# Kernel tuning notes

Measured on AMD Instinct MI355X. Metric: run time of the kernel, lower is better.

## Reference

```python
import jax, jax.numpy as jnp
import numpy as np

N = 50000        # n_nodes
E = 640000       # n_edges
D = 128          # d_model (in_dim == out_dim)
H = 8            # num_heads
DH = D // H      # head dim = 16
EPS = 1e-5


def _batchnorm(x, g, b):
    # BatchNorm1d, training-mode batch statistics (biased variance)
    mu = jnp.mean(x, axis=0)
    var = jnp.mean((x - mu) ** 2, axis=0)
    return (x - mu) * jax.lax.rsqrt(var + EPS) * g + b


def setup_inputs() -> dict:
    key = jax.random.key(0)
    ks = jax.random.split(key, 16)
    s = 0.05
    h = jax.random.normal(ks[0], (N, D), jnp.float32)
    src = jax.random.randint(ks[1], (E,), 0, N)
    # guarantee every node has >= 1 incoming edge (avoids z == 0)
    dst = jnp.concatenate([jnp.arange(N), jax.random.randint(ks[2], (E - N,), 0, N)])
    return {
        "h": h,
        "src": src,
        "dst": dst,
        "WQ": jax.random.normal(ks[3], (D, D), jnp.float32) * s,
        "WK": jax.random.normal(ks[4], (D, D), jnp.float32) * s,
        "WV": jax.random.normal(ks[5], (D, D), jnp.float32) * s,
        "WO": jax.random.normal(ks[6], (D, D), jnp.float32) * s,
        "bO": jnp.zeros((D,), jnp.float32),
        "W1": jax.random.normal(ks[7], (2 * D, D), jnp.float32) * s,
        "b1": jnp.zeros((2 * D,), jnp.float32),
        "W2": jax.random.normal(ks[8], (D, 2 * D), jnp.float32) * s,
        "b2": jnp.zeros((D,), jnp.float32),
        "bn1_g": jnp.ones((D,), jnp.float32),
        "bn1_b": jnp.zeros((D,), jnp.float32),
        "bn2_g": jnp.ones((D,), jnp.float32),
        "bn2_b": jnp.zeros((D,), jnp.float32),
    }


def reference(h, src, dst, WQ, WK, WV, WO, bO, W1, b1, W2, b2, bn1_g, bn1_b, bn2_g, bn2_b):
    n = h.shape[0]
    # projections -> [N, H, DH]
    Q = (h @ WQ.T).reshape(n, H, DH)
    K = (h @ WK.T).reshape(n, H, DH)
    V = (h @ WV.T).reshape(n, H, DH)
    # per-edge score: sum(K[src] * Q[dst]) -> [E, H]; clamp/exp (scaled_exp)
    score = jnp.sum(K[src] * Q[dst], axis=-1) / np.sqrt(DH)
    score = jnp.exp(jnp.clip(score, -5.0, 5.0))
    # scatter-sum weighted values and normalizers to destination nodes
    wV = jax.ops.segment_sum(V[src] * score[..., None], dst, num_segments=n)  # [N,H,DH]
    z = jax.ops.segment_sum(score, dst, num_segments=n)                       # [N,H]
    attn = (wV / z[..., None]).reshape(n, D)
    # O projection + residual + BN1
    h1 = _batchnorm(h + (attn @ WO.T + bO), bn1_g, bn1_b)
    # FFN + residual + BN2
    f = jax.nn.relu(h1 @ W1.T + b1) @ W2.T + b2
    return _batchnorm(h1 + f, bn2_g, bn2_b)
```

## Files before the change

### kernel.cpp

```cpp
#include <hip/hip_runtime.h>
#include <math.h>


#define ND128 16384
typedef _Float16 f16;
typedef __attribute__((ext_vector_type(8))) _Float16 h8;
typedef __attribute__((ext_vector_type(4))) _Float16 h4;
typedef __attribute__((ext_vector_type(2))) _Float16 h2;
typedef __attribute__((ext_vector_type(4))) float f4;
typedef __attribute__((ext_vector_type(2))) float ff2;

__device__ __forceinline__ float fast_exp2(float x) {
#if __has_builtin(__builtin_amdgcn_exp2f)
    return __builtin_amdgcn_exp2f(x);
#else
    return exp2f(x);
#endif
}

template <int CTRL>
__device__ __forceinline__ float dppadd(float x) {
    int t = __builtin_amdgcn_update_dpp(0, __float_as_int(x), CTRL, 0xF, 0xF, false);
    return x + __int_as_float(t);
}
__device__ __forceinline__ float wsum8(float p) {
    p = dppadd<0xB1>(p);
    p = dppadd<0x4E>(p);
    p = dppadd<0x141>(p);
    return p;
}

__device__ __forceinline__ ff2 fp8x2_dec_sw(unsigned v) {
    ff2 r;
    unsigned b0 = v & 0xffu, b1 = (v >> 8) & 0xffu;
    {
        unsigned e = (b0 >> 3) & 15u, m = b0 & 7u;
        float x = e ? __uint_as_float(((e + 120u) << 23) | (m << 20)) : (float)m * 0.001953125f;
        r.x = (b0 & 0x80u) ? -x : x;
    }
    {
        unsigned e = (b1 >> 3) & 15u, m = b1 & 7u;
        float x = e ? __uint_as_float(((e + 120u) << 23) | (m << 20)) : (float)m * 0.001953125f;
        r.y = (b1 & 0x80u) ? -x : x;
    }
    return r;
}

__device__ __forceinline__ ff2 dec_lo(unsigned v) {
#if __has_builtin(__builtin_amdgcn_cvt_pk_f32_fp8)
    return __builtin_amdgcn_cvt_pk_f32_fp8((int)v, false);
#else
    return fp8x2_dec_sw(v & 0xffffu);
#endif
}
__device__ __forceinline__ ff2 dec_hi(unsigned v) {
#if __has_builtin(__builtin_amdgcn_cvt_pk_f32_fp8)
    return __builtin_amdgcn_cvt_pk_f32_fp8((int)v, true);
#else
    return fp8x2_dec_sw((v >> 16) & 0xffffu);
#endif
}

#if !__has_builtin(__builtin_amdgcn_cvt_pk_fp8_f32)
__device__ __forceinline__ unsigned char fp8_1(float f) {
    float a = fabsf(f);
    unsigned sg = (__float_as_uint(f) >> 31) << 7;
    if (a >= 448.f) return (unsigned char)(sg | 0x7E);
    if (a < 0.0009765625f) return (unsigned char)sg;
    int E; float m = frexpf(a, &E);
    if (E - 1 < -6) {
        int q = (int)rintf(a * 512.f);
        if (q > 7) return (unsigned char)(sg | 0x08);
        return (unsigned char)(sg | q);
    }
    int q = (int)rintf(m * 16.f);
    if (q == 16) { q = 8; E += 1; }
    int Ef = E - 1 + 7;
    if (Ef > 15) return (unsigned char)(sg | 0x7E);
    return (unsigned char)(sg | (Ef << 3) | (q - 8));
}
#endif

__device__ __forceinline__ unsigned short fp8_pack2(float a0, float a1) {
#if __has_builtin(__builtin_amdgcn_cvt_pk_fp8_f32)
    int pk = __builtin_amdgcn_cvt_pk_fp8_f32(a0, a1, 0, false);
    return (unsigned short)(pk & 0xffff);
#else
    return (unsigned short)((unsigned)fp8_1(a0) | ((unsigned)fp8_1(a1) << 8));
#endif
}

__global__ __launch_bounds__(256) void k_prep_hist(
    const float* __restrict__ WQ, const float* __restrict__ WK,
    const float* __restrict__ WV, const float* __restrict__ WO,
    const float* __restrict__ W2,
    f16* __restrict__ Wqb, f16* __restrict__ Wkb,
    f16* __restrict__ Wvb, f16* __restrict__ Wob, f16* __restrict__ W2b,
    int* __restrict__ cursor, const int* __restrict__ dst,
    int N, int E, int nhb)
{
    const int tid = threadIdx.x;
    if (blockIdx.x < (unsigned)nhb) {
        int e = blockIdx.x * 256 + tid;
        if (e < E) atomicAdd(&cursor[dst[e]], 1);
        return;
    }
    const int ws = blockIdx.x - nhb;
    const float* Wsrc; f16* dstw; int K, base;
    if (ws < 4) {
        Wsrc = ws == 0 ? WQ : ws == 1 ? WK : ws == 2 ? WV : WO;
        dstw = ws == 0 ? Wqb : ws == 1 ? Wkb : ws == 2 ? Wvb : Wob;
        K = 128; base = 0;
    } else {
        Wsrc = W2; dstw = W2b; K = 256; base = (ws - 4) * 2048;
    }
#pragma unroll
    for (int it = 0; it < 8; ++it) {
        int cid = base + it * 256 + tid;
        int lane = cid & 63;
        int kb, nt;
        if (K == 128) { kb = (cid >> 6) & 3; nt = cid >> 8; }
        else          { kb = (cid >> 6) & 7; nt = cid >> 9; }
        int row = nt * 16 + (lane & 15);
        int col = kb * 32 + (lane >> 4) * 8;
        const float* pp = Wsrc + (size_t)row * K + col;
        f16 o8[8];
#pragma unroll
        for (int j = 0; j < 8; ++j) o8[j] = (f16)pp[j];
        *(h8*)(dstw + (size_t)cid * 8) = *(const h8*)o8;
    }
}

__global__ __launch_bounds__(512) void k_qkvf(
    const float* __restrict__ h, f16* __restrict__ hb,
    const f16* __restrict__ Wqb, const f16* __restrict__ Wkb,
    const f16* __restrict__ Wvb,
    f16* __restrict__ Qb, unsigned char* __restrict__ KV8,
    const int* __restrict__ cursor, int* __restrict__ bsum, int N, int nsb)
{
    __shared__ f16 sA[ND128];
    __shared__ int ws8[8];
    const int tid = threadIdx.x;
    if (blockIdx.x < (unsigned)nsb) {
        int base = blockIdx.x * 2048 + tid * 4;
        int s = 0;
#pragma unroll
        for (int j = 0; j < 4; ++j) {
            int idx = base + j;
            if (idx < N) s += cursor[idx];
        }
#pragma unroll
        for (int off = 32; off; off >>= 1) s += __shfl_down(s, off, 64);
        if ((tid & 63) == 0) ws8[tid >> 6] = s;
        __syncthreads();
        if (tid == 0) {
            int r = 0;
#pragma unroll
            for (int k = 0; k < 8; ++k) r += ws8[k];
            bsum[blockIdx.x] = r;
        }
        return;
    }
    const int slab = blockIdx.x - nsb;
#pragma unroll
    for (int it = 0; it < 4; ++it) {
        int cid = it * 512 + tid;
        int lane = cid & 63;
        int m = (cid >> 6) & 7;
        int kb = cid >> 9;
        int row = slab * 128 + m * 16 + (lane & 15);
        int col = kb * 32 + (lane >> 4) * 8;
        f16 o8[8];
        if (row < N) {
            const float* pp = h + (size_t)row * 128 + col;
            float4 f0 = *(const float4*)pp;
            float4 f1 = *(const float4*)(pp + 4);
            o8[0] = (f16)f0.x; o8[1] = (f16)f0.y; o8[2] = (f16)f0.z; o8[3] = (f16)f0.w;
            o8[4] = (f16)f1.x; o8[5] = (f16)f1.y; o8[6] = (f16)f1.z; o8[7] = (f16)f1.w;
        } else {
#pragma unroll
            for (int j = 0; j < 8; ++j) o8[j] = (f16)0.f;
        }
        h8 v = *(const h8*)o8;
        *(h8*)(hb + (size_t)slab * ND128 + (size_t)cid * 8) = v;
        *(h8*)(sA + (size_t)cid * 8) = v;
    }
    __syncthreads();

    const int w2 = tid >> 6, lane = tid & 63;
    const int rl = lane & 15, quad = lane >> 4;
#pragma unroll
    for (int oidx = 0; oidx < 3; ++oidx) {
        const f16* __restrict__ Wb = oidx == 0 ? Wqb : oidx == 1 ? Wkb : Wvb;
        h8 bfr[4];
#pragma unroll
        for (int kb = 0; kb < 4; ++kb)
            bfr[kb] = *(const h8*)(Wb + (size_t)((w2 * 4 + kb) * 64 + lane) * 8);

        f4 acc[8];
        f4 zero = {0.f, 0.f, 0.f, 0.f};
#pragma unroll
        for (int m = 0; m < 8; ++m) acc[m] = zero;
#pragma unroll
        for (int m = 0; m < 8; ++m) {
#pragma unroll
            for (int kb = 0; kb < 4; ++kb) {
                h8 a = *(const h8*)(sA + (size_t)((kb * 8 + m) * 64 + lane) * 8);
                acc[m] = __builtin_amdgcn_mfma_f32_16x16x32_f16(bfr[kb], a, acc[m], 0, 0, 0);
            }
        }
        if (oidx == 0) {
#pragma unroll
            for (int m = 0; m < 8; ++m) {
                int gr = slab * 128 + m * 16 + rl;
                if (gr < N) {
                    h4 o;
                    o[0] = (f16)acc[m][0]; o[1] = (f16)acc[m][1];
                    o[2] = (f16)acc[m][2]; o[3] = (f16)acc[m][3];
                    *(h4*)(Qb + (size_t)gr * 128 + w2 * 16 + quad * 4) = o;
                }
            }
        } else {
            const int koff = (oidx == 2) ? 2 : 0;
#pragma unroll
            for (int m = 0; m < 8; ++m) {
                int gr = slab * 128 + m * 16 + rl;
                if (gr < N) {
                    int c0 = w2 * 16 + quad * 4;
                    unsigned short p01 = fp8_pack2(acc[m][0], acc[m][1]);
                    unsigned short p23 = fp8_pack2(acc[m][2], acc[m][3]);
                    unsigned char* rowp = KV8 + (size_t)gr * 256 + (size_t)c0 * 2 + koff;
                    *(unsigned short*)(rowp) = p01;
                    *(unsigned short*)(rowp + 4) = p23;
                }
            }
        }
    }
}

__global__ __launch_bounds__(256) void k_scanC(
    const int* __restrict__ cnt, const int* __restrict__ bsum,
    int* __restrict__ rowptr, int* __restrict__ cursor, int N, int nsb)
{
    const int t = threadIdx.x, b = blockIdx.x;
    __shared__ int sboff;
    if (t == 0) {
        int r = 0;
        for (int i2 = 0; i2 < b; ++i2) r += bsum[i2];
        sboff = r;
    }
    if (t == 64 && b == nsb - 1) {
        int r = 0;
        for (int i2 = 0; i2 < nsb; ++i2) r += bsum[i2];
        rowptr[N] = r;
    }
    int base = b * 2048 + t * 8;
    int loc[8];
    int s = 0;
#pragma unroll
    for (int j = 0; j < 8; ++j) {
        int idx = base + j;
        loc[j] = (idx < N) ? cnt[idx] : 0;
        s += loc[j];
    }
    __shared__ int part[256];
    part[t] = s;
    __syncthreads();
    for (int off = 1; off < 256; off <<= 1) {
        int v = (t >= off) ? part[t - off] : 0;
        __syncthreads();
        part[t] += v;
        __syncthreads();
    }
    int run = sboff + (t ? part[t - 1] : 0);
#pragma unroll
    for (int j = 0; j < 8; ++j) {
        int idx = base + j;
        if (idx < N) { rowptr[idx] = run; cursor[idx] = run; run += loc[j]; }
    }
}

__global__ __launch_bounds__(256) void k_scatter(
    const int* __restrict__ src, const int* __restrict__ dst,
    int* __restrict__ cursor, int* __restrict__ csr_src, int E)
{
    int e = blockIdx.x * 256 + threadIdx.x;
    if (e < E) {
        int pos = atomicAdd(&cursor[dst[e]], 1);
        csr_src[pos] = src[e];
    }
}

__global__ __launch_bounds__(256) void k_attn(
    const f16* __restrict__ Qb, const unsigned char* __restrict__ KV8,
    const int* __restrict__ rowptr, const int* __restrict__ csr_src,
    f16* __restrict__ attnf, int N)
{
    const int node = blockIdx.x * 4 + (threadIdx.x >> 6);
    const int lane = threadIdx.x & 63;
    if (node >= N) return;
    const int beg = rowptr[node], end = rowptr[node + 1];

    float qx, qy;
    {
        h2 q2 = ((const h2*)(Qb + (size_t)node * 128))[lane];
        const float SCL = 0.25f * 1.44269504f;
        qx = (float)q2[0] * SCL;
        qy = (float)q2[1] * SCL;
    }
    const float CLP = 5.f * 1.44269504f;
    const unsigned loff = 4u * (unsigned)lane;

    float axA = 0.f, ayA = 0.f, axB = 0.f, ayB = 0.f, zA = 0.f, zB = 0.f;
    int i = beg;
    for (; i + 7 < end; i += 8) {
        int s[8];
#pragma unroll
        for (int u = 0; u < 8; ++u) s[u] = csr_src[i + u];
        unsigned kv[8];
#pragma unroll
        for (int u = 0; u < 8; ++u)
            kv[u] = *(const unsigned*)(KV8 + (size_t)s[u] * 256 + loff);
        float p[8];
#pragma unroll
        for (int u = 0; u < 8; ++u) {
            ff2 kf = dec_lo(kv[u]);
            p[u] = fmaf(qx, kf.x, qy * kf.y);
        }
#pragma unroll
        for (int u = 0; u < 8; ++u) p[u] = wsum8(p[u]);
        float sc[8];
#pragma unroll
        for (int u = 0; u < 8; ++u)
            sc[u] = fast_exp2(fminf(fmaxf(p[u], -CLP), CLP));
#pragma unroll
        for (int u = 0; u < 8; ++u) {
            ff2 vf = dec_hi(kv[u]);
            if (u & 1) {
                axB = fmaf(vf.x, sc[u], axB); ayB = fmaf(vf.y, sc[u], ayB); zB += sc[u];
            } else {
                axA = fmaf(vf.x, sc[u], axA); ayA = fmaf(vf.y, sc[u], ayA); zA += sc[u];
            }
        }
    }
    if (i + 3 < end) {
        int s[4];
#pragma unroll
        for (int u = 0; u < 4; ++u) s[u] = csr_src[i + u];
        unsigned kv[4];
#pragma unroll
        for (int u = 0; u < 4; ++u)
            kv[u] = *(const unsigned*)(KV8 + (size_t)s[u] * 256 + loff);
#pragma unroll
        for (int u = 0; u < 4; ++u) {
            ff2 kf = dec_lo(kv[u]);
            float p = wsum8(fmaf(qx, kf.x, qy * kf.y));
            float scu = fast_exp2(fminf(fmaxf(p, -CLP), CLP));
            ff2 vf = dec_hi(kv[u]);
            if (u & 1) {
                axB = fmaf(vf.x, scu, axB); ayB = fmaf(vf.y, scu, ayB); zB += scu;
            } else {
                axA = fmaf(vf.x, scu, axA); ayA = fmaf(vf.y, scu, ayA); zA += scu;
            }
        }
        i += 4;
    }
    for (; i < end; ++i) {
        int s0 = csr_src[i];
        unsigned kv = *(const unsigned*)(KV8 + (size_t)s0 * 256 + loff);
        ff2 kf = dec_lo(kv);
        float p0 = wsum8(fmaf(qx, kf.x, qy * kf.y));
        float sc0 = fast_exp2(fminf(fmaxf(p0, -CLP), CLP));
        ff2 vf = dec_hi(kv);
        axA = fmaf(vf.x, sc0, axA); ayA = fmaf(vf.y, sc0, ayA);
        zA += sc0;
    }
    float inv = 1.f / (zA + zB);
    h2 o2;
    o2[0] = (f16)((axA + axB) * inv);
    o2[1] = (f16)((ayA + ayB) * inv);
    int slab = node >> 7, m = (node >> 4) & 7, lr = node & 15;
    int kb = lane >> 4, quad2 = (lane & 15) >> 2, j = (lane & 3) * 2;
    *(h2*)(attnf + (size_t)slab * ND128 +
           (size_t)(((kb * 8 + m) * 64 + lr + 16 * quad2) * 8 + j)) = o2;
}

__global__ __launch_bounds__(256) void k_oproj(
    const f16* __restrict__ attnf, const f16* __restrict__ Wob,
    const f16* __restrict__ hbf, const float* __restrict__ bO,
    f16* __restrict__ t1b, float* __restrict__ bn, int N)
{
    __shared__ float csum[128], csq[128];
    const int tid = threadIdx.x, slab = blockIdx.x;
    const int w = tid >> 6, lane = tid & 63;
    if (tid < 128) { csum[tid] = 0.f; csq[tid] = 0.f; }
    __syncthreads();
    const f16* A = attnf + (size_t)slab * ND128;
    const f16* HB = hbf + (size_t)slab * ND128;

    h8 bfr[2][4];
#pragma unroll
    for (int nt = 0; nt < 2; ++nt)
#pragma unroll
        for (int kb = 0; kb < 4; ++kb)
            bfr[nt][kb] = *(const h8*)(Wob + (size_t)(((2 * w + nt) * 4 + kb) * 64 + lane) * 8);

    f4 acc[8][2];
    f4 zero = {0.f, 0.f, 0.f, 0.f};
#pragma unroll
    for (int m = 0; m < 8; ++m) { acc[m][0] = zero; acc[m][1] = zero; }
#pragma unroll
    for (int m = 0; m < 8; ++m) {
#pragma unroll
        for (int kb = 0; kb < 4; ++kb) {
            h8 a = *(const h8*)(A + (size_t)((kb * 8 + m) * 64 + lane) * 8);
            acc[m][0] = __builtin_amdgcn_mfma_f32_16x16x32_f16(bfr[0][kb], a, acc[m][0], 0, 0, 0);
            acc[m][1] = __builtin_amdgcn_mfma_f32_16x16x32_f16(bfr[1][kb], a, acc[m][1], 0, 0, 0);
        }
    }

    const int rl = lane & 15, quad = lane >> 4;
    float4 bo[2];
#pragma unroll
    for (int nt = 0; nt < 2; ++nt)
        bo[nt] = *(const float4*)(bO + w * 32 + nt * 16 + quad * 4);
    float pcs[2][4], pcq[2][4];
#pragma unroll
    for (int nt = 0; nt < 2; ++nt)
#pragma unroll
        for (int r = 0; r < 4; ++r) { pcs[nt][r] = 0.f; pcq[nt][r] = 0.f; }

#pragma unroll
    for (int m = 0; m < 8; ++m) {
        int gr = slab * 128 + m * 16 + rl;
        if (gr < N) {
#pragma unroll
            for (int nt = 0; nt < 2; ++nt) {
                size_t fidx = (size_t)(((w * 8 + m) * 64 + (nt * 2 + (quad >> 1)) * 16 + rl) * 8 +
                                       (quad & 1) * 4);
                h4 hv4 = *(const h4*)(HB + fidx);
                float v0 = acc[m][nt][0] + (float)hv4[0] + bo[nt].x;
                float v1 = acc[m][nt][1] + (float)hv4[1] + bo[nt].y;
                float v2 = acc[m][nt][2] + (float)hv4[2] + bo[nt].z;
                float v3 = acc[m][nt][3] + (float)hv4[3] + bo[nt].w;
                h4 o; o[0] = (f16)v0; o[1] = (f16)v1; o[2] = (f16)v2; o[3] = (f16)v3;
                *(h4*)(t1b + (size_t)slab * ND128 + fidx) = o;
                pcs[nt][0] += v0; pcq[nt][0] += v0 * v0;
                pcs[nt][1] += v1; pcq[nt][1] += v1 * v1;
                pcs[nt][2] += v2; pcq[nt][2] += v2 * v2;
                pcs[nt][3] += v3; pcq[nt][3] += v3 * v3;
            }
        }
    }
#pragma unroll
    for (int nt = 0; nt < 2; ++nt)
#pragma unroll
        for (int r = 0; r < 4; ++r) {
            float s = pcs[nt][r], q = pcq[nt][r];
            s += __shfl_xor(s, 8, 16); q += __shfl_xor(q, 8, 16);
            s += __shfl_xor(s, 4, 16); q += __shfl_xor(q, 4, 16);
            s += __shfl_xor(s, 2, 16); q += __shfl_xor(q, 2, 16);
            s += __shfl_xor(s, 1, 16); q += __shfl_xor(q, 1, 16);
            if (rl == 0) {
                int cl = w * 32 + nt * 16 + quad * 4 + r;
                atomicAdd(&csum[cl], s);
                atomicAdd(&csq[cl], q);
            }
        }
    __syncthreads();
    if (tid < 128) {
        atomicAdd(bn + tid, csum[tid]);
        atomicAdd(bn + 128 + tid, csq[tid]);
    }
}

__global__ __launch_bounds__(128) void k_fold1(
    const float* __restrict__ bn, const float* __restrict__ g1,
    const float* __restrict__ bb1, const float* __restrict__ W1,
    const float* __restrict__ b1, f16* __restrict__ W1b,
    float* __restrict__ badj, float* __restrict__ sfold,
    float* __restrict__ bfold, int N)
{
    const int o = blockIdx.x, i = threadIdx.x;
    float invN = 1.f / (float)N;
    float mu = bn[i] * invN;
    float var = bn[128 + i] * invN - mu * mu;
    float s = g1[i] * rsqrtf(var + 1e-5f);
    float bb = bb1[i] - mu * s;
    if (o == 0) { sfold[i] = s; bfold[i] = bb; }
    float wv = W1[(size_t)o * 128 + i];
    __shared__ float red[128];
    red[i] = wv * bb;
    const int nt = o >> 4, lanelow = o & 15;
    const int kb = i >> 5, quad = (i >> 3) & 3, j = i & 7;
    W1b[(size_t)(((nt * 4 + kb) * 64 + lanelow + 16 * quad) * 8 + j)] = (f16)(wv * s);
    __syncthreads();
#pragma unroll
    for (int off = 64; off; off >>= 1) {
        if (i < off) red[i] += red[i + off];
        __syncthreads();
    }
    if (i == 0) badj[o] = b1[o] + red[0];
}

__global__ __launch_bounds__(256) void k_ffn1(
    const f16* __restrict__ t1b, const f16* __restrict__ W1b,
    const float* __restrict__ badj, f16* __restrict__ ub, int N)
{
    const int slab = blockIdx.x, ch = blockIdx.y;
    const int w = threadIdx.x >> 6, lane = threadIdx.x & 63;
    const f16* A = t1b + (size_t)slab * ND128;

    h8 bfr[2][4];
#pragma unroll
    for (int nt = 0; nt < 2; ++nt)
#pragma unroll
        for (int kb = 0; kb < 4; ++kb) {
            int ntg = ch * 8 + 2 * w + nt;
            bfr[nt][kb] = *(const h8*)(W1b + (size_t)((ntg * 4 + kb) * 64 + lane) * 8);
        }

    f4 acc[8][2];
    f4 zero = {0.f, 0.f, 0.f, 0.f};
#pragma unroll
    for (int m = 0; m < 8; ++m) { acc[m][0] = zero; acc[m][1] = zero; }
#pragma unroll
    for (int m = 0; m < 8; ++m) {
#pragma unroll
        for (int kb = 0; kb < 4; ++kb) {
            h8 a = *(const h8*)(A + (size_t)((kb * 8 + m) * 64 + lane) * 8);
            acc[m][0] = __builtin_amdgcn_mfma_f32_16x16x32_f16(bfr[0][kb], a, acc[m][0], 0, 0, 0);
            acc[m][1] = __builtin_amdgcn_mfma_f32_16x16x32_f16(bfr[1][kb], a, acc[m][1], 0, 0, 0);
        }
    }

    const int rl = lane & 15, quad = lane >> 4;
    const int kbu = ch * 4 + w;
    float4 ba[2];
#pragma unroll
    for (int nt = 0; nt < 2; ++nt)
        ba[nt] = *(const float4*)(badj + ch * 128 + w * 32 + nt * 16 + quad * 4);
#pragma unroll
    for (int m = 0; m < 8; ++m) {
        int gr = slab * 128 + m * 16 + rl;
        if (gr < N) {
#pragma unroll
            for (int nt = 0; nt < 2; ++nt) {
                h4 o;
                o[0] = (f16)fmaxf(acc[m][nt][0] + ba[nt].x, 0.f);
                o[1] = (f16)fmaxf(acc[m][nt][1] + ba[nt].y, 0.f);
                o[2] = (f16)fmaxf(acc[m][nt][2] + ba[nt].z, 0.f);
                o[3] = (f16)fmaxf(acc[m][nt][3] + ba[nt].w, 0.f);
                *(h4*)(ub + (size_t)slab * 32768 +
                       (size_t)(((kbu * 8 + m) * 64 + (nt * 2 + (quad >> 1)) * 16 + rl) * 8 +
                                (quad & 1) * 4)) = o;
            }
        }
    }
}

__global__ __launch_bounds__(256) void k_ffn2(
    const f16* __restrict__ ub, const f16* __restrict__ W2b,
    const f16* __restrict__ t1b,
    const float* __restrict__ sfold, const float* __restrict__ bfold,
    const float* __restrict__ b2, f16* __restrict__ t2f,
    float* __restrict__ bn, int N)
{
    __shared__ float csum[128], csq[128], sS[128], sB[128];
    const int tid = threadIdx.x, slab = blockIdx.x;
    const int w = tid >> 6, lane = tid & 63;
    if (tid < 128) {
        csum[tid] = 0.f; csq[tid] = 0.f;
        sS[tid] = sfold[tid]; sB[tid] = bfold[tid] + b2[tid];
    }
    __syncthreads();
    const f16* A = ub + (size_t)slab * 32768;
    const f16* T1 = t1b + (size_t)slab * ND128;

    h8 bfr[2][8];
#pragma unroll
    for (int nt = 0; nt < 2; ++nt)
#pragma unroll
        for (int kb = 0; kb < 8; ++kb)
            bfr[nt][kb] = *(const h8*)(W2b + (size_t)(((2 * w + nt) * 8 + kb) * 64 + lane) * 8);

    f4 acc[8][2];
    f4 zero = {0.f, 0.f, 0.f, 0.f};
#pragma unroll
    for (int m = 0; m < 8; ++m) { acc[m][0] = zero; acc[m][1] = zero; }
#pragma unroll
    for (int m = 0; m < 8; ++m) {
#pragma unroll
        for (int kb = 0; kb < 8; ++kb) {
            h8 a = *(const h8*)(A + (size_t)((kb * 8 + m) * 64 + lane) * 8);
            acc[m][0] = __builtin_amdgcn_mfma_f32_16x16x32_f16(bfr[0][kb], a, acc[m][0], 0, 0, 0);
            acc[m][1] = __builtin_amdgcn_mfma_f32_16x16x32_f16(bfr[1][kb], a, acc[m][1], 0, 0, 0);
        }
    }

    const int rl = lane & 15, quad = lane >> 4;
    float pcs[2][4], pcq[2][4];
#pragma unroll
    for (int nt = 0; nt < 2; ++nt)
#pragma unroll
        for (int r = 0; r < 4; ++r) { pcs[nt][r] = 0.f; pcq[nt][r] = 0.f; }

#pragma unroll
    for (int m = 0; m < 8; ++m) {
        int gr = slab * 128 + m * 16 + rl;
        if (gr < N) {
#pragma unroll
            for (int nt = 0; nt < 2; ++nt) {
                int col0 = w * 32 + nt * 16 + quad * 4;
                size_t fidx = (size_t)(((w * 8 + m) * 64 + (nt * 2 + (quad >> 1)) * 16 + rl) * 8 +
                                       (quad & 1) * 4);
                h4 t1v = *(const h4*)(T1 + fidx);
                float4 ss = *(const float4*)&sS[col0];
                float4 sb = *(const float4*)&sB[col0];
                h4 o2;
                o2[0] = (f16)(acc[m][nt][0] + fmaf(ss.x, (float)t1v[0], sb.x));
                o2[1] = (f16)(acc[m][nt][1] + fmaf(ss.y, (float)t1v[1], sb.y));
                o2[2] = (f16)(acc[m][nt][2] + fmaf(ss.z, (float)t1v[2], sb.z));
                o2[3] = (f16)(acc[m][nt][3] + fmaf(ss.w, (float)t1v[3], sb.w));
                *(h4*)(t2f + (size_t)slab * ND128 + fidx) = o2;
                float r0 = (float)o2[0], r1 = (float)o2[1];
                float r2 = (float)o2[2], r3 = (float)o2[3];
                pcs[nt][0] += r0; pcq[nt][0] += r0 * r0;
                pcs[nt][1] += r1; pcq[nt][1] += r1 * r1;
                pcs[nt][2] += r2; pcq[nt][2] += r2 * r2;
                pcs[nt][3] += r3; pcq[nt][3] += r3 * r3;
            }
        }
    }
#pragma unroll
    for (int nt = 0; nt < 2; ++nt)
#pragma unroll
        for (int r = 0; r < 4; ++r) {
            float s = pcs[nt][r], q = pcq[nt][r];
            s += __shfl_xor(s, 8, 16); q += __shfl_xor(q, 8, 16);
            s += __shfl_xor(s, 4, 16); q += __shfl_xor(q, 4, 16);
            s += __shfl_xor(s, 2, 16); q += __shfl_xor(q, 2, 16);
            s += __shfl_xor(s, 1, 16); q += __shfl_xor(q, 1, 16);
            if (rl == 0) {
                int cl = w * 32 + nt * 16 + quad * 4 + r;
                atomicAdd(&csum[cl], s);
                atomicAdd(&csq[cl], q);
            }
        }
    __syncthreads();
    if (tid < 128) {
        atomicAdd(bn + 256 + tid, csum[tid]);
        atomicAdd(bn + 384 + tid, csq[tid]);
    }
}

__global__ __launch_bounds__(256) void k_bn2(
    const f16* __restrict__ t2f, float* __restrict__ out,
    const float* __restrict__ bn,
    const float* __restrict__ g2, const float* __restrict__ bb2, int N)
{
    __shared__ float sS[128], sB[128];
    const int tid = threadIdx.x;
    if (tid < 128) {
        float invN = 1.f / (float)N;
        float mu = bn[256 + tid] * invN;
        float var = bn[384 + tid] * invN - mu * mu;
        float scl = g2[tid] * rsqrtf(var + 1e-5f);
        sS[tid] = scl;
        sB[tid] = bb2[tid] - mu * scl;
    }
    __syncthreads();
    size_t idx = (size_t)blockIdx.x * 256 + tid;
    size_t total = (size_t)N * 32;
    if (idx < total) {
        int gr = (int)(idx >> 5);
        int c0 = ((int)idx & 31) * 4;
        int slab = gr >> 7, m = (gr >> 4) & 7, rl = gr & 15;
        int w = c0 >> 5, nt = (c0 >> 4) & 1, q = (c0 >> 2) & 3;
        size_t fidx = (size_t)(((w * 8 + m) * 64 + (nt * 2 + (q >> 1)) * 16 + rl) * 8 +
                               (q & 1) * 4);
        h4 v = *(const h4*)(t2f + (size_t)slab * ND128 + fidx);
        float4 o;
        o.x = fmaf((float)v[0], sS[c0 + 0], sB[c0 + 0]);
        o.y = fmaf((float)v[1], sS[c0 + 1], sB[c0 + 1]);
        o.z = fmaf((float)v[2], sS[c0 + 2], sB[c0 + 2]);
        o.w = fmaf((float)v[3], sS[c0 + 3], sB[c0 + 3]);
        *(float4*)(out + (size_t)gr * 128 + c0) = o;
    }
}

extern "C" void kernel_launch(void* const* d_in, const int* in_sizes, int n_in,
                              void* d_out, int out_size, void* d_ws, size_t ws_size,
                              hipStream_t stream)
{
    const float* h   = (const float*)d_in[0];
    const int*   src = (const int*)d_in[1];
    const int*   dst = (const int*)d_in[2];
    const float* WQ  = (const float*)d_in[3];
    const float* WK  = (const float*)d_in[4];
    const float* WV  = (const float*)d_in[5];
    const float* WO  = (const float*)d_in[6];
    const float* bO  = (const float*)d_in[7];
    const float* W1  = (const float*)d_in[8];
    const float* b1  = (const float*)d_in[9];
    const float* W2  = (const float*)d_in[10];
    const float* b2  = (const float*)d_in[11];
    const float* g1  = (const float*)d_in[12];
    const float* bb1 = (const float*)d_in[13];
    const float* g2  = (const float*)d_in[14];
    const float* bb2 = (const float*)d_in[15];
    float* out = (float*)d_out;

    int N = in_sizes[0] / 128;
    int E = in_sizes[1];
    int slabs = (N + 127) / 128;
    int nsb = (N + 2047) / 2048;
    int nhb = (E + 255) / 256;
    const size_t B1 = (size_t)slabs * 32768;

    char* Wp = (char*)d_ws;
    f16* hb  = (f16*)Wp;
    f16* Qb  = (f16*)(Wp + B1);
    unsigned char* KV8 = (unsigned char*)(Wp + 2 * B1);
    f16* attnf = (f16*)(Wp + 3 * B1);
    f16* t1b = (f16*)(Wp + 4 * B1);
    f16* ub  = (f16*)(Wp + B1);
    f16* t2f = attnf;
    const size_t base = 5 * B1;
    f16* Wqb = (f16*)(Wp + base);
    f16* Wkb = (f16*)(Wp + base + 32768);
    f16* Wvb = (f16*)(Wp + base + 65536);
    f16* Wob = (f16*)(Wp + base + 98304);
    f16* W1b = (f16*)(Wp + base + 131072);
    f16* W2b = (f16*)(Wp + base + 196608);
    float* badj  = (float*)(Wp + base + 262144);
    float* sfold = (float*)(Wp + base + 263168);
    float* bfold = (float*)(Wp + base + 263680);
    float* bn    = (float*)(Wp + base + 264192);
    int* bsum    = (int*)(Wp + base + 266240);
    int* cursor  = (int*)(Wp + base + 266496);
    int* rowptr  = (int*)(Wp + base + 266496 + (size_t)N * 4);
    int* csr     = (int*)(Wp + base + 266496 + (size_t)N * 8 + 8);

    hipMemsetAsync(Wp + base + 264192, 0, 2304 + (size_t)N * 4, stream);
    k_prep_hist<<<nhb + 6, 256, 0, stream>>>(
        WQ, WK, WV, WO, W2, Wqb, Wkb, Wvb, Wob, W2b, cursor, dst, N, E, nhb);
    k_qkvf<<<nsb + slabs, 512, 0, stream>>>(
        h, hb, Wqb, Wkb, Wvb, Qb, KV8, cursor, bsum, N, nsb);
    k_scanC<<<nsb, 256, 0, stream>>>(cursor, bsum, rowptr, cursor, N, nsb);
    k_scatter<<<nhb, 256, 0, stream>>>(src, dst, cursor, csr, E);
    k_attn<<<(N + 3) / 4, 256, 0, stream>>>(Qb, KV8, rowptr, csr, attnf, N);
    k_oproj<<<slabs, 256, 0, stream>>>(attnf, Wob, hb, bO, t1b, bn, N);
    k_fold1<<<256, 128, 0, stream>>>(bn, g1, bb1, W1, b1, W1b, badj, sfold, bfold, N);
    k_ffn1<<<dim3(slabs, 2), 256, 0, stream>>>(t1b, W1b, badj, ub, N);
    k_ffn2<<<slabs, 256, 0, stream>>>(ub, W2b, t1b, sfold, bfold, b2, t2f, bn, N);
    k_bn2<<<(int)(((size_t)N * 32 + 255) / 256), 256, 0, stream>>>(t2f, out, bn, g2, bb2, N);
}
```

Baseline: 298.2 us.

## Fuse FFN up and down projections into one kernel with LDS intermediate

Merges the two FFN GEMM kernels into a single 512-thread kernel per 128-row slab. The ReLU hidden activations are kept in 64KB of shared memory instead of being written to and reread from global memory, which removes one launch and that round trip. The per-block shared-memory reduction of the BN2 statistics is dropped in favour of direct global atomics from each wave. The large LDS footprint limits blocks per CU, and the extra global atomics add contention.

```diff
diff --git a/kernel.cpp b/kernel.cpp
--- a/kernel.cpp
+++ b/kernel.cpp
@@ -503,47 +503,47 @@
     if (i == 0) badj[o] = b1[o] + red[0];
 }
 
-__global__ __launch_bounds__(256) void k_ffn1(
+__global__ __launch_bounds__(512) void k_ffn(
     const f16* __restrict__ t1b, const f16* __restrict__ W1b,
-    const float* __restrict__ badj, f16* __restrict__ ub, int N)
-{
-    const int slab = blockIdx.x, ch = blockIdx.y;
-    const int w = threadIdx.x >> 6, lane = threadIdx.x & 63;
-    const f16* A = t1b + (size_t)slab * ND128;
-
-    h8 bfr[2][4];
-#pragma unroll
-    for (int nt = 0; nt < 2; ++nt)
-#pragma unroll
-        for (int kb = 0; kb < 4; ++kb) {
-            int ntg = ch * 8 + 2 * w + nt;
-            bfr[nt][kb] = *(const h8*)(W1b + (size_t)((ntg * 4 + kb) * 64 + lane) * 8);
-        }
-
-    f4 acc[8][2];
-    f4 zero = {0.f, 0.f, 0.f, 0.f};
-#pragma unroll
-    for (int m = 0; m < 8; ++m) { acc[m][0] = zero; acc[m][1] = zero; }
-#pragma unroll
-    for (int m = 0; m < 8; ++m) {
-#pragma unroll
-        for (int kb = 0; kb < 4; ++kb) {
-            h8 a = *(const h8*)(A + (size_t)((kb * 8 + m) * 64 + lane) * 8);
-            acc[m][0] = __builtin_amdgcn_mfma_f32_16x16x32_f16(bfr[0][kb], a, acc[m][0], 0, 0, 0);
-            acc[m][1] = __builtin_amdgcn_mfma_f32_16x16x32_f16(bfr[1][kb], a, acc[m][1], 0, 0, 0);
-        }
-    }
-
+    const float* __restrict__ badj, const f16* __restrict__ W2b,
+    const float* __restrict__ sfold, const float* __restrict__ bfold,
+    const float* __restrict__ b2, f16* __restrict__ t2f,
+    float* __restrict__ bn, int N)
+{
+    __shared__ f16 uf[32768];
+    const int tid = threadIdx.x, slab = blockIdx.x;
+    const int w2 = tid >> 6, lane = tid & 63;
     const int rl = lane & 15, quad = lane >> 4;
-    const int kbu = ch * 4 + w;
-    float4 ba[2];
-#pragma unroll
-    for (int nt = 0; nt < 2; ++nt)
-        ba[nt] = *(const float4*)(badj + ch * 128 + w * 32 + nt * 16 + quad * 4);
-#pragma unroll
-    for (int m = 0; m < 8; ++m) {
-        int gr = slab * 128 + m * 16 + rl;
-        if (gr < N) {
+    const f16* T1 = t1b + (size_t)slab * ND128;
+
+    {
+        h8 bfr[2][4];
+#pragma unroll
+        for (int nt = 0; nt < 2; ++nt) {
+            int ntg = w2 * 2 + nt;
+#pragma unroll
+            for (int kb = 0; kb < 4; ++kb)
+                bfr[nt][kb] = *(const h8*)(W1b + (size_t)((ntg * 4 + kb) * 64 + lane) * 8);
+        }
+        f4 acc[8][2];
+        f4 zero = {0.f, 0.f, 0.f, 0.f};
+#pragma unroll
+        for (int m = 0; m < 8; ++m) { acc[m][0] = zero; acc[m][1] = zero; }
+#pragma unroll
+        for (int m = 0; m < 8; ++m) {
+#pragma unroll
+            for (int kb = 0; kb < 4; ++kb) {
+                h8 a = *(const h8*)(T1 + (size_t)((kb * 8 + m) * 64 + lane) * 8);
+                acc[m][0] = __builtin_amdgcn_mfma_f32_16x16x32_f16(bfr[0][kb], a, acc[m][0], 0, 0, 0);
+                acc[m][1] = __builtin_amdgcn_mfma_f32_16x16x32_f16(bfr[1][kb], a, acc[m][1], 0, 0, 0);
+            }
+        }
+        float4 ba[2];
+#pragma unroll
+        for (int nt = 0; nt < 2; ++nt)
+            ba[nt] = *(const float4*)(badj + (w2 * 2 + nt) * 16 + quad * 4);
+#pragma unroll
+        for (int m = 0; m < 8; ++m) {
 #pragma unroll
             for (int nt = 0; nt < 2; ++nt) {
                 h4 o;
@@ -551,106 +551,76 @@
                 o[1] = (f16)fmaxf(acc[m][nt][1] + ba[nt].y, 0.f);
                 o[2] = (f16)fmaxf(acc[m][nt][2] + ba[nt].z, 0.f);
                 o[3] = (f16)fmaxf(acc[m][nt][3] + ba[nt].w, 0.f);
-                *(h4*)(ub + (size_t)slab * 32768 +
-                       (size_t)(((kbu * 8 + m) * 64 + (nt * 2 + (quad >> 1)) * 16 + rl) * 8 +
-                                (quad & 1) * 4)) = o;
-            }
-        }
-    }
-}
-
-__global__ __launch_bounds__(256) void k_ffn2(
-    const f16* __restrict__ ub, const f16* __restrict__ W2b,
-    const f16* __restrict__ t1b,
-    const float* __restrict__ sfold, const float* __restrict__ bfold,
-    const float* __restrict__ b2, f16* __restrict__ t2f,
-    float* __restrict__ bn, int N)
-{
-    __shared__ float csum[128], csq[128], sS[128], sB[128];
-    const int tid = threadIdx.x, slab = blockIdx.x;
-    const int w = tid >> 6, lane = tid & 63;
-    if (tid < 128) {
-        csum[tid] = 0.f; csq[tid] = 0.f;
-        sS[tid] = sfold[tid]; sB[tid] = bfold[tid] + b2[tid];
+                *(h4*)(uf + (size_t)(((w2 * 8 + m) * 64 +
+                       (nt * 2 + (quad >> 1)) * 16 + rl) * 8 + (quad & 1) * 4)) = o;
+            }
+        }
     }
     __syncthreads();
-    const f16* A = ub + (size_t)slab * 32768;
-    const f16* T1 = t1b + (size_t)slab * ND128;
-
-    h8 bfr[2][8];
-#pragma unroll
-    for (int nt = 0; nt < 2; ++nt)
+
+    {
+        h8 bfr2[8];
 #pragma unroll
         for (int kb = 0; kb < 8; ++kb)
-            bfr[nt][kb] = *(const h8*)(W2b + (size_t)(((2 * w + nt) * 8 + kb) * 64 + lane) * 8);
-
-    f4 acc[8][2];
-    f4 zero = {0.f, 0.f, 0.f, 0.f};
-#pragma unroll
-    for (int m = 0; m < 8; ++m) { acc[m][0] = zero; acc[m][1] = zero; }
-#pragma unroll
-    for (int m = 0; m < 8; ++m) {
-#pragma unroll
-        for (int kb = 0; kb < 8; ++kb) {
-            h8 a = *(const h8*)(A + (size_t)((kb * 8 + m) * 64 + lane) * 8);
-            acc[m][0] = __builtin_amdgcn_mfma_f32_16x16x32_f16(bfr[0][kb], a, acc[m][0], 0, 0, 0);
-            acc[m][1] = __builtin_amdgcn_mfma_f32_16x16x32_f16(bfr[1][kb], a, acc[m][1], 0, 0, 0);
-        }
-    }
-
-    const int rl = lane & 15, quad = lane >> 4;
-    float pcs[2][4], pcq[2][4];
-#pragma unroll
-    for (int nt = 0; nt < 2; ++nt)
-#pragma unroll
-        for (int r = 0; r < 4; ++r) { pcs[nt][r] = 0.f; pcq[nt][r] = 0.f; }
-
-#pragma unroll
-    for (int m = 0; m < 8; ++m) {
-        int gr = slab * 128 + m * 16 + rl;
-        if (gr < N) {
-#pragma unroll
-            for (int nt = 0; nt < 2; ++nt) {
-                int col0 = w * 32 + nt * 16 + quad * 4;
-                size_t fidx = (size_t)(((w * 8 + m) * 64 + (nt * 2 + (quad >> 1)) * 16 + rl) * 8 +
-                                       (quad & 1) * 4);
+            bfr2[kb] = *(const h8*)(W2b + (size_t)((w2 * 8 + kb) * 64 + lane) * 8);
+
+        f4 acc2[8];
+        f4 zero = {0.f, 0.f, 0.f, 0.f};
+#pragma unroll
+        for (int m = 0; m < 8; ++m) acc2[m] = zero;
+#pragma unroll
+        for (int m = 0; m < 8; ++m) {
+#pragma unroll
+            for (int kb = 0; kb < 8; ++kb) {
+                h8 a = *(const h8*)(uf + (size_t)((kb * 8 + m) * 64 + lane) * 8);
+                acc2[m] = __builtin_amdgcn_mfma_f32_16x16x32_f16(bfr2[kb], a, acc2[m], 0, 0, 0);
+            }
+        }
+
+        const int c0 = w2 * 16 + quad * 4;
+        float4 ss = *(const float4*)(sfold + c0);
+        float4 sbA = *(const float4*)(bfold + c0);
+        float4 sbB = *(const float4*)(b2 + c0);
+        float4 sb;
+        sb.x = sbA.x + sbB.x; sb.y = sbA.y + sbB.y;
+        sb.z = sbA.z + sbB.z; sb.w = sbA.w + sbB.w;
+
+        float pcs[4] = {0.f, 0.f, 0.f, 0.f};
+        float pcq[4] = {0.f, 0.f, 0.f, 0.f};
+#pragma unroll
+        for (int m = 0; m < 8; ++m) {
+            int gr = slab * 128 + m * 16 + rl;
+            if (gr < N) {
+                size_t fidx = (size_t)((((w2 >> 1) * 8 + m) * 64 +
+                              ((w2 & 1) * 2 + (quad >> 1)) * 16 + rl) * 8 + (quad & 1) * 4);
                 h4 t1v = *(const h4*)(T1 + fidx);
-                float4 ss = *(const float4*)&sS[col0];
-                float4 sb = *(const float4*)&sB[col0];
                 h4 o2;
-                o2[0] = (f16)(acc[m][nt][0] + fmaf(ss.x, (float)t1v[0], sb.x));
-                o2[1] = (f16)(acc[m][nt][1] + fmaf(ss.y, (float)t1v[1], sb.y));
-                o2[2] = (f16)(acc[m][nt][2] + fmaf(ss.z, (float)t1v[2], sb.z));
-                o2[3] = (f16)(acc[m][nt][3] + fmaf(ss.w, (float)t1v[3], sb.w));
+                o2[0] = (f16)(acc2[m][0] + fmaf(ss.x, (float)t1v[0], sb.x));
+                o2[1] = (f16)(acc2[m][1] + fmaf(ss.y, (float)t1v[1], sb.y));
+                o2[2] = (f16)(acc2[m][2] + fmaf(ss.z, (float)t1v[2], sb.z));
+                o2[3] = (f16)(acc2[m][3] + fmaf(ss.w, (float)t1v[3], sb.w));
                 *(h4*)(t2f + (size_t)slab * ND128 + fidx) = o2;
                 float r0 = (float)o2[0], r1 = (float)o2[1];
                 float r2 = (float)o2[2], r3 = (float)o2[3];
-                pcs[nt][0] += r0; pcq[nt][0] += r0 * r0;
-                pcs[nt][1] += r1; pcq[nt][1] += r1 * r1;
-                pcs[nt][2] += r2; pcq[nt][2] += r2 * r2;
-                pcs[nt][3] += r3; pcq[nt][3] += r3 * r3;
-            }
-        }
-    }
-#pragma unroll
-    for (int nt = 0; nt < 2; ++nt)
+                pcs[0] += r0; pcq[0] += r0 * r0;
+                pcs[1] += r1; pcq[1] += r1 * r1;
+                pcs[2] += r2; pcq[2] += r2 * r2;
+                pcs[3] += r3; pcq[3] += r3 * r3;
+            }
+        }
 #pragma unroll
         for (int r = 0; r < 4; ++r) {
-            float s = pcs[nt][r], q = pcq[nt][r];
+            float s = pcs[r], q = pcq[r];
             s += __shfl_xor(s, 8, 16); q += __shfl_xor(q, 8, 16);
             s += __shfl_xor(s, 4, 16); q += __shfl_xor(q, 4, 16);
             s += __shfl_xor(s, 2, 16); q += __shfl_xor(q, 2, 16);
             s += __shfl_xor(s, 1, 16); q += __shfl_xor(q, 1, 16);
             if (rl == 0) {
-                int cl = w * 32 + nt * 16 + quad * 4 + r;
-                atomicAdd(&csum[cl], s);
-                atomicAdd(&csq[cl], q);
-            }
-        }
-    __syncthreads();
-    if (tid < 128) {
-        atomicAdd(bn + 256 + tid, csum[tid]);
-        atomicAdd(bn + 384 + tid, csq[tid]);
+                int cl = c0 + r;
+                atomicAdd(bn + 256 + cl, s);
+                atomicAdd(bn + 384 + cl, q);
+            }
+        }
     }
 }
 
@@ -724,7 +694,6 @@
     unsigned char* KV8 = (unsigned char*)(Wp + 2 * B1);
     f16* attnf = (f16*)(Wp + 3 * B1);
     f16* t1b = (f16*)(Wp + 4 * B1);
-    f16* ub  = (f16*)(Wp + B1);
     f16* t2f = attnf;
     const size_t base = 5 * B1;
     f16* Wqb = (f16*)(Wp + base);
@@ -752,7 +721,6 @@
     k_attn<<<(N + 3) / 4, 256, 0, stream>>>(Qb, KV8, rowptr, csr, attnf, N);
     k_oproj<<<slabs, 256, 0, stream>>>(attnf, Wob, hb, bO, t1b, bn, N);
     k_fold1<<<256, 128, 0, stream>>>(bn, g1, bb1, W1, b1, W1b, badj, sfold, bfold, N);
-    k_ffn1<<<dim3(slabs, 2), 256, 0, stream>>>(t1b, W1b, badj, ub, N);
-    k_ffn2<<<slabs, 256, 0, stream>>>(ub, W2b, t1b, sfold, bfold, b2, t2f, bn, N);
+    k_ffn<<<slabs, 512, 0, stream>>>(t1b, W1b, badj, W2b, sfold, bfold, b2, t2f, bn, N);
     k_bn2<<<(int)(((size_t)N * 32 + 255) / 256), 256, 0, stream>>>(t2f, out, bn, g2, bb2, N);
 }
```

Result: slower. 313.1 us (+5.0%).
